# Performance work log

Measured on AMD Instinct MI355X. Metric: run time of the kernel, lower is better.

## Reference

```python
import jax, jax.numpy as jnp
import numpy as np

N_NODES = 100000

def gcn_conv(x, W, b, src, dst):
    n = x.shape[0]
    loop = jnp.arange(n, dtype=src.dtype)
    src_f = jnp.concatenate([src, loop])
    dst_f = jnp.concatenate([dst, loop])
    deg = jax.ops.segment_sum(jnp.ones_like(src_f, dtype=x.dtype), dst_f, num_segments=n)
    dinv = jnp.where(deg > 0, deg ** -0.5, 0.0)
    norm = dinv[src_f] * dinv[dst_f]              # [E+N]
    h = x @ W                                      # [N, out]
    msg = h[src_f] * norm[:, None]                 # gather + scale
    out = jax.ops.segment_sum(msg, dst_f, num_segments=n)
    return out + b

def setup_inputs() -> dict:
    key = jax.random.key(0)
    k1, k2, k3, k4, k5 = jax.random.split(key, 5)
    d = 128
    x = jax.random.normal(k1, (N_NODES, d), dtype=jnp.float32)
    e = jax.random.randint(k2, (2, 3200000), 0, N_NODES, dtype=jnp.int64)
    # Glorot-style init as in PyG GCNConv
    W1 = jax.random.normal(k3, (d, 64), dtype=jnp.float32) * (1.0 / np.sqrt(d))
    b1 = jnp.zeros((64,), dtype=jnp.float32)
    W2 = jax.random.normal(k4, (64, 1), dtype=jnp.float32) * (1.0 / np.sqrt(64))
    b2 = jnp.zeros((1,), dtype=jnp.float32)
    return {"x": x, "e": e, "W1": W1, "b1": b1, "W2": W2, "b2": b2}

def reference(x, e, W1, b1, W2, b2):
    src, dst = e[0], e[1]
    h = jax.nn.relu(gcn_conv(x, W1, b1, src, dst))
    return gcn_conv(h, W2, b2, src, dst)
```

## Files before the change

### kernel.cpp

```cpp
#include <hip/hip_runtime.h>
#include <hip/hip_bf16.h>


typedef short s8_t __attribute__((ext_vector_type(8)));
typedef float f4_t __attribute__((ext_vector_type(4)));

__device__ __forceinline__ float bf2f(unsigned short u) {
    union { unsigned int u; float f; } c; c.u = ((unsigned int)u) << 16; return c.f;
}
__device__ __forceinline__ unsigned short f2bf(float f) {
    union { float f; unsigned int u; } c; c.f = f;
    unsigned int u = c.u;
    unsigned int r = (u + 0x7fffu + ((u >> 16) & 1u)) >> 16;
    return (unsigned short)r;
}
__device__ __forceinline__ float loadF(const void* p, int i, int isbf) {
    return isbf ? bf2f(((const unsigned short*)p)[i]) : ((const float*)p)[i];
}
__device__ __forceinline__ int edgeIdx(const void* e, long long i, int is64) {
    return is64 ? (int)((const long long*)e)[i] : ((const int*)e)[i];
}

__global__ void k_detect(const void* e, const void* x, int* flags) {
    int lane = threadIdx.x;
    unsigned int ew = ((const unsigned int*)e)[2 * lane + 1];
    unsigned long long nz = __ballot(ew != 0);
    unsigned int xw = ((const unsigned int*)x)[lane];
    unsigned int low = xw & 0xffffu;
    unsigned int e8 = (low >> 7) & 0xffu;
    bool plaus = (low == 0u) || (e8 >= 110u && e8 <= 135u);
    unsigned long long pl = __ballot(plaus);
    if (lane == 0) {
        flags[0] = (nz == 0ull) ? 1 : 0;
        flags[1] = (__popcll(pl) > 32) ? 1 : 0;
    }
}

__global__ void k_prep_all(const void* W1, unsigned short* __restrict__ wT,
                           unsigned short* __restrict__ wTh,
                           unsigned short* __restrict__ wTl, const int* flags) {
    int tid = threadIdx.x;
    if (flags[1]) {
        const unsigned short* w = (const unsigned short*)W1;
        for (int idx = tid; idx < 128 * 64; idx += 256) {
            int k = idx >> 6, n = idx & 63;
            wT[n * 128 + k] = w[idx];
        }
    } else {
        const float* w = (const float*)W1;
        for (int idx = tid; idx < 128 * 64; idx += 256) {
            int k = idx >> 6, n = idx & 63;
            float v = w[idx];
            unsigned short h = f2bf(v);
            wTh[n * 128 + k] = h;
            wTl[n * 128 + k] = f2bf(v - bf2f(h));
        }
    }
}

__launch_bounds__(256)
__global__ void k_hist(const void* e, int* __restrict__ histT, const int* flags,
                       int E, int B, int HB) {
    __shared__ int hist[1024];
    int tid = threadIdx.x;
    int is64 = flags[0];
    for (int f = tid; f < B; f += 256) hist[f] = 0;
    __syncthreads();
    int base = blockIdx.x * 4096;
    #pragma unroll
    for (int k = 0; k < 16; ++k) {
        int i = base + k * 256 + tid;
        if (i < E) {
            int d = edgeIdx(e, (long long)E + i, is64);
            atomicAdd(&hist[d >> 9], 1);
        }
    }
    __syncthreads();
    for (int f = tid; f < B; f += 256)
        histT[(long long)f * HB + blockIdx.x] = hist[f];
}

__global__ void k_scanA(int* __restrict__ data, int* __restrict__ partial, int M) {
    __shared__ int s[256];
    int tid = threadIdx.x;
    int i = blockIdx.x * 256 + tid;
    int v = (i < M) ? data[i] : 0;
    s[tid] = v; __syncthreads();
    for (int off = 1; off < 256; off <<= 1) {
        int t = (tid >= off) ? s[tid - off] : 0;
        __syncthreads(); s[tid] += t; __syncthreads();
    }
    if (i < M) data[i] = s[tid] - v;
    if (tid == 255) partial[blockIdx.x] = s[255];
}

__global__ void k_scanB(int* __restrict__ partial, int nP) {
    __shared__ int s[1024];
    int tid = threadIdx.x;
    int C = (nP + 1023) >> 10;
    int base = tid * C;
    int v[8]; int tot = 0;
    for (int j = 0; j < C; ++j) { v[j] = (base + j < nP) ? partial[base + j] : 0; tot += v[j]; }
    s[tid] = tot; __syncthreads();
    for (int off = 1; off < 1024; off <<= 1) {
        int t = (tid >= off) ? s[tid - off] : 0;
        __syncthreads(); s[tid] += t; __syncthreads();
    }
    int run = s[tid] - tot;
    for (int j = 0; j < C; ++j) { if (base + j < nP) { int tmp = v[j]; partial[base + j] = run; run += tmp; } }
}

__global__ void k_scanC(int* __restrict__ data, const int* __restrict__ partial,
                        int* __restrict__ bucketStart, int M, int HB, int B, int E) {
    int f = blockIdx.x * 256 + threadIdx.x;
    if (f < M) {
        int val = data[f] + partial[f >> 8];
        data[f] = val;
        int q = f / HB;
        if (f - q * HB == 0) bucketStart[q] = val;
    }
    if (f == 0) bucketStart[B] = E;
}

__launch_bounds__(256)
__global__ void k_part(const void* e, const int* __restrict__ histT,
                       int* __restrict__ part, const int* flags,
                       int E, int B, int HB) {
    __shared__ int lcur[1024];
    int tid = threadIdx.x;
    int is64 = flags[0];
    for (int f = tid; f < B; f += 256)
        lcur[f] = histT[(long long)f * HB + blockIdx.x];
    __syncthreads();
    int base = blockIdx.x * 4096;
    #pragma unroll
    for (int k = 0; k < 16; ++k) {
        int i = base + k * 256 + tid;
        if (i < E) {
            int s = edgeIdx(e, i, is64);
            int d = edgeIdx(e, (long long)E + i, is64);
            int pos = atomicAdd(&lcur[d >> 9], 1);
            part[pos] = s | ((d & 511) << 17);
        }
    }
}

__launch_bounds__(512)
__global__ void k_sort2(const int* __restrict__ part, const int* __restrict__ bucketStart,
                        int* __restrict__ srcSorted, int* __restrict__ start,
                        float* __restrict__ dinv, int N, int B) {
    __shared__ int cnt[512];
    __shared__ int s[512];
    __shared__ int cur[512];
    int tid = threadIdx.x, b = blockIdx.x;
    cnt[tid] = 0;
    __syncthreads();
    int lo = bucketStart[b], hi = bucketStart[b + 1];
    for (int idx = lo + tid; idx < hi; idx += 512)
        atomicAdd(&cnt[(part[idx] >> 17) & 511], 1);
    __syncthreads();
    int v = cnt[tid];
    s[tid] = v; __syncthreads();
    for (int off = 1; off < 512; off <<= 1) {
        int t = (tid >= off) ? s[tid - off] : 0;
        __syncthreads(); s[tid] += t; __syncthreads();
    }
    int base_ = lo + s[tid] - v;
    cur[tid] = base_;
    int node = b * 512 + tid;
    if (node < N) {
        start[node] = base_;
        dinv[node] = rsqrtf((float)(v + 1));
    }
    if (b == 0 && tid == 0) start[N] = bucketStart[B];
    __syncthreads();
    for (int idx = lo + tid; idx < hi; idx += 512) {
        int pw = part[idx];
        int pos = atomicAdd(&cur[(pw >> 17) & 511], 1);
        srcSorted[pos] = pw & 0x1FFFF;
    }
}

__launch_bounds__(256)
__global__ void k_gemm(const void* x, const unsigned short* __restrict__ wT,
                       const unsigned short* __restrict__ wTh,
                       const unsigned short* __restrict__ wTl,
                       const float* __restrict__ dinv,
                       unsigned short* __restrict__ hb, const int* flags, int N) {
    int tid = threadIdx.x;
    int lane = tid & 63, wv = tid >> 6;
    int q = lane >> 4, r = lane & 15;
    int gw = blockIdx.x * 4 + wv;
    int nW = gridDim.x * 4;
    int RB = (N + 15) >> 4;
    int isbf = flags[1];
    if (isbf) {
        const unsigned short* xb = (const unsigned short*)x;
        for (int rb = gw; rb < RB; rb += nW) {
            int row0 = rb * 16;
            int arow = row0 + r;
            s8_t a[4];
            #pragma unroll
            for (int kk = 0; kk < 4; ++kk)
                a[kk] = (arow < N)
                    ? *(const s8_t*)&xb[(long long)arow * 128 + kk * 32 + q * 8]
                    : (s8_t)(short)0;
            f4_t acc[4];
            #pragma unroll
            for (int nt = 0; nt < 4; ++nt) acc[nt] = (f4_t){0.f, 0.f, 0.f, 0.f};
            #pragma unroll
            for (int nt = 0; nt < 4; ++nt) {
                #pragma unroll
                for (int kk = 0; kk < 4; ++kk) {
                    s8_t b = *(const s8_t*)&wT[(nt * 16 + r) * 128 + kk * 32 + q * 8];
                    acc[nt] = __builtin_amdgcn_mfma_f32_16x16x32_bf16(a[kk], b, acc[nt], 0, 0, 0);
                }
            }
            #pragma unroll
            for (int reg = 0; reg < 4; ++reg) {
                int row = row0 + q * 4 + reg;
                if (row < N) {
                    float dv = dinv[row];
                    #pragma unroll
                    for (int nt = 0; nt < 4; ++nt)
                        hb[(long long)row * 64 + nt * 16 + r] = f2bf(acc[nt][reg] * dv);
                }
            }
        }
    } else {
        const float* xf = (const float*)x;
        f4_t cx0[4], cx1[4];
        int rb = gw;
        if (rb < RB) {
            int arow = rb * 16 + r;
            #pragma unroll
            for (int kk = 0; kk < 4; ++kk) {
                if (arow < N) {
                    const float* p = &xf[(long long)arow * 128 + kk * 32 + q * 8];
                    cx0[kk] = *(const f4_t*)p;
                    cx1[kk] = *(const f4_t*)(p + 4);
                } else {
                    cx0[kk] = (f4_t){0.f, 0.f, 0.f, 0.f};
                    cx1[kk] = (f4_t){0.f, 0.f, 0.f, 0.f};
                }
            }
        }
        for (; rb < RB; rb += nW) {
            s8_t ah[4], al[4];
            #pragma unroll
            for (int kk = 0; kk < 4; ++kk) {
                #pragma unroll
                for (int j = 0; j < 4; ++j) {
                    union { float f; unsigned int u; } c0, h0, r0, c1, h1, r1;
                    c0.f = cx0[kk][j];
                    h0.u = c0.u & 0xffff0000u;
                    ah[kk][j] = (short)(c0.u >> 16);
                    r0.f = c0.f - h0.f;
                    al[kk][j] = (short)(r0.u >> 16);
                    c1.f = cx1[kk][j];
                    h1.u = c1.u & 0xffff0000u;
                    ah[kk][4 + j] = (short)(c1.u >> 16);
                    r1.f = c1.f - h1.f;
                    al[kk][4 + j] = (short)(r1.u >> 16);
                }
            }
            int rbn = rb + nW;
            if (rbn < RB) {
                int arow = rbn * 16 + r;
                #pragma unroll
                for (int kk = 0; kk < 4; ++kk) {
                    if (arow < N) {
                        const float* p = &xf[(long long)arow * 128 + kk * 32 + q * 8];
                        cx0[kk] = *(const f4_t*)p;
                        cx1[kk] = *(const f4_t*)(p + 4);
                    } else {
                        cx0[kk] = (f4_t){0.f, 0.f, 0.f, 0.f};
                        cx1[kk] = (f4_t){0.f, 0.f, 0.f, 0.f};
                    }
                }
            }
            f4_t acc[4];
            #pragma unroll
            for (int nt = 0; nt < 4; ++nt) acc[nt] = (f4_t){0.f, 0.f, 0.f, 0.f};
            #pragma unroll
            for (int nt = 0; nt < 4; ++nt) {
                #pragma unroll
                for (int kk = 0; kk < 4; ++kk) {
                    s8_t bh = *(const s8_t*)&wTh[(nt * 16 + r) * 128 + kk * 32 + q * 8];
                    s8_t bl = *(const s8_t*)&wTl[(nt * 16 + r) * 128 + kk * 32 + q * 8];
                    acc[nt] = __builtin_amdgcn_mfma_f32_16x16x32_bf16(ah[kk], bh, acc[nt], 0, 0, 0);
                    acc[nt] = __builtin_amdgcn_mfma_f32_16x16x32_bf16(al[kk], bh, acc[nt], 0, 0, 0);
                    acc[nt] = __builtin_amdgcn_mfma_f32_16x16x32_bf16(ah[kk], bl, acc[nt], 0, 0, 0);
                }
            }
            int row0 = rb * 16;
            #pragma unroll
            for (int reg = 0; reg < 4; ++reg) {
                int row = row0 + q * 4 + reg;
                if (row < N) {
                    float dv = dinv[row];
                    #pragma unroll
                    for (int nt = 0; nt < 4; ++nt)
                        hb[(long long)row * 64 + nt * 16 + r] = f2bf(acc[nt][reg] * dv);
                }
            }
        }
    }
}

__launch_bounds__(256)
__global__ void k_agg1(const unsigned short* __restrict__ hb,
                       const float* __restrict__ dinv,
                       const int* __restrict__ start,
                       const int* __restrict__ srcSorted,
                       const void* b1, const void* W2, float* __restrict__ sbuf2,
                       const int* flags, int N) {
    int lane = threadIdx.x & 63;
    int node = (blockIdx.x * blockDim.x + threadIdx.x) >> 6;
    if (node >= N) return;
    int isbf = flags[1];
    float di = dinv[node];
    int base = start[node], cnt = start[node + 1] - base;
    float acc = bf2f(hb[(long long)node * 64 + lane]);
    for (int c = 0; c < cnt; c += 64) {
        int t = c + lane;
        int sidx = (t < cnt) ? srcSorted[base + t] : 0;
        int m = cnt - c; if (m > 64) m = 64;
        int t2 = 0;
        for (; t2 + 16 <= m; t2 += 16) {
            int s0  = __shfl(sidx, t2 + 0),  s1  = __shfl(sidx, t2 + 1);
            int s2  = __shfl(sidx, t2 + 2),  s3  = __shfl(sidx, t2 + 3);
            int s4  = __shfl(sidx, t2 + 4),  s5  = __shfl(sidx, t2 + 5);
            int s6  = __shfl(sidx, t2 + 6),  s7  = __shfl(sidx, t2 + 7);
            int s8  = __shfl(sidx, t2 + 8),  s9  = __shfl(sidx, t2 + 9);
            int s10 = __shfl(sidx, t2 + 10), s11 = __shfl(sidx, t2 + 11);
            int s12 = __shfl(sidx, t2 + 12), s13 = __shfl(sidx, t2 + 13);
            int s14 = __shfl(sidx, t2 + 14), s15 = __shfl(sidx, t2 + 15);
            unsigned short v0  = hb[(long long)s0  * 64 + lane];
            unsigned short v1  = hb[(long long)s1  * 64 + lane];
            unsigned short v2  = hb[(long long)s2  * 64 + lane];
            unsigned short v3  = hb[(long long)s3  * 64 + lane];
            unsigned short v4  = hb[(long long)s4  * 64 + lane];
            unsigned short v5  = hb[(long long)s5  * 64 + lane];
            unsigned short v6  = hb[(long long)s6  * 64 + lane];
            unsigned short v7  = hb[(long long)s7  * 64 + lane];
            unsigned short v8  = hb[(long long)s8  * 64 + lane];
            unsigned short v9  = hb[(long long)s9  * 64 + lane];
            unsigned short v10 = hb[(long long)s10 * 64 + lane];
            unsigned short v11 = hb[(long long)s11 * 64 + lane];
            unsigned short v12 = hb[(long long)s12 * 64 + lane];
            unsigned short v13 = hb[(long long)s13 * 64 + lane];
            unsigned short v14 = hb[(long long)s14 * 64 + lane];
            unsigned short v15 = hb[(long long)s15 * 64 + lane];
            acc += bf2f(v0);  acc += bf2f(v1);  acc += bf2f(v2);  acc += bf2f(v3);
            acc += bf2f(v4);  acc += bf2f(v5);  acc += bf2f(v6);  acc += bf2f(v7);
            acc += bf2f(v8);  acc += bf2f(v9);  acc += bf2f(v10); acc += bf2f(v11);
            acc += bf2f(v12); acc += bf2f(v13); acc += bf2f(v14); acc += bf2f(v15);
        }
        for (; t2 + 8 <= m; t2 += 8) {
            int s0 = __shfl(sidx, t2 + 0), s1 = __shfl(sidx, t2 + 1);
            int s2 = __shfl(sidx, t2 + 2), s3 = __shfl(sidx, t2 + 3);
            int s4 = __shfl(sidx, t2 + 4), s5 = __shfl(sidx, t2 + 5);
            int s6 = __shfl(sidx, t2 + 6), s7 = __shfl(sidx, t2 + 7);
            unsigned short v0 = hb[(long long)s0 * 64 + lane];
            unsigned short v1 = hb[(long long)s1 * 64 + lane];
            unsigned short v2 = hb[(long long)s2 * 64 + lane];
            unsigned short v3 = hb[(long long)s3 * 64 + lane];
            unsigned short v4 = hb[(long long)s4 * 64 + lane];
            unsigned short v5 = hb[(long long)s5 * 64 + lane];
            unsigned short v6 = hb[(long long)s6 * 64 + lane];
            unsigned short v7 = hb[(long long)s7 * 64 + lane];
            acc += bf2f(v0); acc += bf2f(v1); acc += bf2f(v2); acc += bf2f(v3);
            acc += bf2f(v4); acc += bf2f(v5); acc += bf2f(v6); acc += bf2f(v7);
        }
        for (; t2 < m; ++t2) {
            int s0 = __shfl(sidx, t2);
            acc += bf2f(hb[(long long)s0 * 64 + lane]);
        }
    }
    float v = acc * di + loadF(b1, lane, isbf);
    v = fmaxf(v, 0.f);
    float p = v * loadF(W2, lane, isbf);
    #pragma unroll
    for (int o = 32; o >= 1; o >>= 1) p += __shfl_xor(p, o);
    if (lane == 0) sbuf2[node] = p * di;
}

__launch_bounds__(256)
__global__ void k_agg2(const float* __restrict__ sbuf2, const float* __restrict__ dinv,
                       const int* __restrict__ start,
                       const int* __restrict__ srcSorted,
                       const void* b2, void* out, const int* flags, int N) {
    int lane = threadIdx.x & 63;
    int node = (blockIdx.x * blockDim.x + threadIdx.x) >> 6;
    if (node >= N) return;
    int isbf = flags[1];
    float di = dinv[node];
    int base = start[node], cnt = start[node + 1] - base;
    float part = 0.f;
    for (int t = lane; t < cnt; t += 64) part += sbuf2[srcSorted[base + t]];
    #pragma unroll
    for (int o = 32; o >= 1; o >>= 1) part += __shfl_xor(part, o);
    if (lane == 0) {
        float o_ = (part + sbuf2[node]) * di + loadF(b2, 0, isbf);
        if (isbf) ((unsigned short*)out)[node] = f2bf(o_);
        else      ((float*)out)[node] = o_;
    }
}

extern "C" void kernel_launch(void* const* d_in, const int* in_sizes, int n_in,
                              void* d_out, int out_size, void* d_ws, size_t ws_size,
                              hipStream_t stream) {
    const void* x  = d_in[0];
    const void* e  = d_in[1];
    const void* W1 = d_in[2];
    const void* b1 = d_in[3];
    const void* W2 = d_in[4];
    const void* b2 = d_in[5];
    int N = in_sizes[0] / 128;
    int E = in_sizes[1] / 2;
    int B  = (N + 511) / 512;
    int HB = (E + 4095) / 4096;
    int M  = B * HB;
    int nP = (M + 255) / 256;
    int NB = B * 512;
    int EP = ((E + 255) / 256) * 256;

    int*   wsI         = (int*)d_ws;
    int*   flags       = wsI;
    unsigned short* wT  = (unsigned short*)(wsI + 256);
    unsigned short* wTh = (unsigned short*)(wsI + 256 + 4096);
    unsigned short* wTl = (unsigned short*)(wsI + 256 + 8192);
    int*   histT       = wsI + 256 + 12288;
    int*   partial     = histT + ((M + 255) / 256) * 256;
    int*   bucketStart = partial + ((nP + 255) / 256) * 256;
    float* dinv        = (float*)(bucketStart + 1040);
    float* sbuf2       = dinv + NB;
    int*   start       = (int*)(sbuf2 + NB);
    int*   srcSorted   = start + NB + 256;
    int*   part        = srcSorted + EP;
    unsigned short* hb = (unsigned short*)part;

    hipLaunchKernelGGL(k_detect, dim3(1), dim3(64), 0, stream, e, x, flags);
    hipLaunchKernelGGL(k_prep_all, dim3(1), dim3(256), 0, stream, W1, wT, wTh, wTl, flags);
    hipLaunchKernelGGL(k_hist, dim3(HB), dim3(256), 0, stream, e, histT, flags, E, B, HB);
    hipLaunchKernelGGL(k_scanA, dim3(nP), dim3(256), 0, stream, histT, partial, M);
    hipLaunchKernelGGL(k_scanB, dim3(1), dim3(1024), 0, stream, partial, nP);
    hipLaunchKernelGGL(k_scanC, dim3(nP), dim3(256), 0, stream,
                       histT, partial, bucketStart, M, HB, B, E);
    hipLaunchKernelGGL(k_part, dim3(HB), dim3(256), 0, stream, e, histT, part, flags, E, B, HB);
    hipLaunchKernelGGL(k_sort2, dim3(B), dim3(512), 0, stream,
                       part, bucketStart, srcSorted, start, dinv, N, B);
    hipLaunchKernelGGL(k_gemm, dim3(512), dim3(256), 0, stream,
                       x, wT, wTh, wTl, dinv, hb, flags, N);
    hipLaunchKernelGGL(k_agg1, dim3((N + 3) / 4), dim3(256), 0, stream,
                       hb, dinv, start, srcSorted, b1, W2, sbuf2, flags, N);
    hipLaunchKernelGGL(k_agg2, dim3((N + 3) / 4), dim3(256), 0, stream,
                       sbuf2, dinv, start, srcSorted, b2, d_out, flags, N);
}
```

Baseline: 313.4 us.

## Stage partition scatter through shared memory for coalesced bucket writes

The partition kernel now ranks each edge within its bucket in shared memory, prefix-scans the per-block bucket counts, and places the packed edges in a local bucket-sorted buffer. It then writes to global memory in sorted order, so consecutive threads store to contiguous addresses within each bucket rather than scattering at random. The cost is about 30KB of extra LDS per block, an in-block scan with several barriers, and extra registers for the per-thread arrays, which may lower occupancy.

```diff
diff --git a/kernel.cpp b/kernel.cpp
--- a/kernel.cpp
+++ b/kernel.cpp
@@ -127,21 +127,60 @@
                        int* __restrict__ part, const int* flags,
                        int E, int B, int HB) {
     __shared__ int lcur[1024];
+    __shared__ int lcnt[1024];
+    __shared__ int sc[256];
+    __shared__ int buf[4096];
+    __shared__ unsigned short bkt[4096];
     int tid = threadIdx.x;
     int is64 = flags[0];
-    for (int f = tid; f < B; f += 256)
-        lcur[f] = histT[(long long)f * HB + blockIdx.x];
+    for (int f = tid; f < 1024; f += 256) {
+        lcur[f] = (f < B) ? histT[(long long)f * HB + blockIdx.x] : 0;
+        lcnt[f] = 0;
+    }
     __syncthreads();
     int base = blockIdx.x * 4096;
+    int val[16], bk[16], rk[16];
     #pragma unroll
     for (int k = 0; k < 16; ++k) {
         int i = base + k * 256 + tid;
         if (i < E) {
             int s = edgeIdx(e, i, is64);
             int d = edgeIdx(e, (long long)E + i, is64);
-            int pos = atomicAdd(&lcur[d >> 9], 1);
-            part[pos] = s | ((d & 511) << 17);
-        }
+            val[k] = s | ((d & 511) << 17);
+            bk[k] = d >> 9;
+            rk[k] = atomicAdd(&lcnt[bk[k]], 1);
+        } else {
+            bk[k] = -1;
+        }
+    }
+    __syncthreads();
+    int c0 = lcnt[4 * tid], c1 = lcnt[4 * tid + 1];
+    int c2 = lcnt[4 * tid + 2], c3 = lcnt[4 * tid + 3];
+    int tot = c0 + c1 + c2 + c3;
+    sc[tid] = tot; __syncthreads();
+    for (int off = 1; off < 256; off <<= 1) {
+        int t = (tid >= off) ? sc[tid - off] : 0;
+        __syncthreads(); sc[tid] += t; __syncthreads();
+    }
+    int run = sc[tid] - tot;
+    lcnt[4 * tid]     = run;
+    lcnt[4 * tid + 1] = run + c0;
+    lcnt[4 * tid + 2] = run + c0 + c1;
+    lcnt[4 * tid + 3] = run + c0 + c1 + c2;
+    __syncthreads();
+    #pragma unroll
+    for (int k = 0; k < 16; ++k) {
+        if (bk[k] >= 0) {
+            int slot = lcnt[bk[k]] + rk[k];
+            buf[slot] = val[k];
+            bkt[slot] = (unsigned short)bk[k];
+        }
+    }
+    __syncthreads();
+    int total = E - base; if (total > 4096) total = 4096;
+    for (int t = tid; t < total; t += 256) {
+        int bb = bkt[t];
+        part[lcur[bb] + (t - lcnt[bb])] = buf[t];
     }
 }
 
```

New measurement: 302.6 us. 3.4% less time.
